# Kernel tuning notes

Measured on AMD Instinct MI355X. Metric: run time of the kernel, lower is better.

Reference implementation:

```python
import jax, jax.numpy as jnp
import numpy as np

T, H, I, E, K, G, TG = 8192, 2048, 1024, 64, 8, 8, 4
ROUTED_SCALE = 2.5


def setup_inputs() -> dict:
    key = jax.random.key(0)
    ks = jax.random.split(key, 7)
    s = 0.02  # weight init scale
    return {
        "hidden_states": jax.random.normal(ks[0], (T, H), jnp.float32),
        "gate_w": jax.random.normal(ks[1], (E, H), jnp.float32) * s,
        "e_bias": jax.random.normal(ks[2], (E,), jnp.float32) * s,
        "w_gate_up": jax.random.normal(ks[3], (E, H, 2 * I), jnp.float32) * s,
        "w_down": jax.random.normal(ks[4], (E, I, H), jnp.float32) * s,
        "shared_gate_up": jax.random.normal(ks[5], (H, 2 * I), jnp.float32) * s,
        "shared_down": jax.random.normal(ks[6], (I, H), jnp.float32) * s,
    }


def silu_and_mul(x):
    g, u = jnp.split(x, 2, axis=-1)
    return jax.nn.silu(g) * u


def grouped_topk(router_logits, e_bias):
    # sigmoid scoring with e_score_correction_bias (DeepSeek-V3 / GLM4-MoE style)
    scores = jax.nn.sigmoid(router_logits)            # [T, E]
    scores_for_choice = scores + e_bias[None, :]
    # group score = sum of top-2 biased scores in each group
    grp = scores_for_choice.reshape(-1, G, E // G)
    group_scores = jax.lax.top_k(grp, 2)[0].sum(-1)   # [T, G]
    _, gidx = jax.lax.top_k(group_scores, TG)         # [T, TG]
    tok = jnp.arange(scores.shape[0])[:, None]
    group_mask = jnp.zeros_like(group_scores, dtype=bool).at[tok, gidx].set(True)
    expert_mask = jnp.repeat(group_mask, E // G, axis=-1)  # [T, E]
    masked = jnp.where(expert_mask, scores_for_choice, -jnp.inf)
    _, topk_ids = jax.lax.top_k(masked, K)            # [T, K]
    # combine weights come from the *unbiased* sigmoid scores
    topk_w = jnp.take_along_axis(scores, topk_ids, axis=-1)
    topk_w = topk_w / jnp.sum(topk_w, axis=-1, keepdims=True)  # renormalize
    return topk_w, topk_ids


def reference(hidden_states, gate_w, e_bias, w_gate_up, w_down,
              shared_gate_up, shared_down):
    x = hidden_states                                  # [T, H]
    # gate runs in fp32
    router_logits = x.astype(jnp.float32) @ gate_w.T   # [T, E]
    topk_w, topk_ids = grouped_topk(router_logits, e_bias)

    # shared expert MLP
    shared_out = silu_and_mul(x @ shared_gate_up) @ shared_down  # [T, H]

    # dense [T, E] combine matrix (top-k sparse in values)
    tok = jnp.arange(x.shape[0])[:, None]
    route = jnp.zeros((x.shape[0], E), x.dtype).at[tok, topk_ids].set(
        topk_w.astype(x.dtype))

    # grouped expert GEMMs via scan over experts (bounds peak memory)
    def body(acc, params):
        w1, w2, rw = params                            # [H,2I], [I,H], [T]
        y = silu_and_mul(x @ w1) @ w2                  # [T, H]
        return acc + rw[:, None] * y, None

    acc0 = jnp.zeros_like(x)
    routed_out, _ = jax.lax.scan(body, acc0, (w_gate_up, w_down, route.T))

    return routed_out * ROUTED_SCALE + shared_out
```

## Files before the change

kernel.cpp:

```cpp
#include <hip/hip_runtime.h>
#include <stdint.h>

#define T_TOK 8192
#define HDIM  2048
#define IDIM  1024
#define NEXP  64
#define KTOP  8
#define TGRP  4
#define TKTOT (T_TOK*KTOP)
#define MAXTILES 1024
#define RSCALE 2.5f

typedef __attribute__((ext_vector_type(8))) short short8;
typedef __attribute__((ext_vector_type(4))) float f32x4;

__device__ __forceinline__ float bf2f(uint16_t u) {
    union { unsigned i; float f; } v; v.i = ((unsigned)u) << 16; return v.f;
}
__device__ __forceinline__ uint16_t f2bf(float f) {
    union { float f; unsigned i; } v; v.f = f;
    unsigned r = (v.i + 0x7FFFu + ((v.i >> 16) & 1u)) >> 16;
    return (uint16_t)r;
}
__device__ __forceinline__ void gload_lds16(const void* g, void* l) {
    __builtin_amdgcn_global_load_lds(
        (const __attribute__((address_space(1))) void*)g,
        (__attribute__((address_space(3))) void*)l, 16, 0, 0);
}
__device__ __forceinline__ int imin(int a, int b) { return a < b ? a : b; }

__global__ __launch_bounds__(256) void k_router(
    const float* __restrict__ x, const float* __restrict__ gw,
    const float* __restrict__ ebias,
    int* __restrict__ topk_ids, float* __restrict__ topk_w,
    int* __restrict__ counts)
{
    __shared__ float xs[16][132];
    __shared__ float wsb[64][133];
    __shared__ float sc[16][65];
    __shared__ float su[16][65];
    const int tid = threadIdx.x;
    const int e = tid & 63;
    const int tg = tid >> 6;
    const long tblk = (long)blockIdx.x * 16;

    float acc0 = 0.f, acc1 = 0.f, acc2 = 0.f, acc3 = 0.f;
    for (int ch = 0; ch < 16; ++ch) {
        const int h0 = ch << 7;
        for (int i = tid; i < 512; i += 256) {
            int r = i >> 5, c4 = (i & 31) << 2;
            float4 v = *(const float4*)(x + (tblk + r) * HDIM + h0 + c4);
            *(float4*)&xs[r][c4] = v;
        }
        for (int i = tid; i < 8192; i += 256) {
            int r = i >> 7, c = i & 127;
            wsb[r][c] = gw[(long)r * HDIM + h0 + c];
        }
        __syncthreads();
        #pragma unroll 8
        for (int hh = 0; hh < 128; ++hh) {
            float wv = wsb[e][hh];
            acc0 += xs[tg][hh] * wv;
            acc1 += xs[tg + 4][hh] * wv;
            acc2 += xs[tg + 8][hh] * wv;
            acc3 += xs[tg + 12][hh] * wv;
        }
        __syncthreads();
    }
    const float be = ebias[e];
    {
        float s;
        s = 1.f / (1.f + expf(-acc0)); su[tg][e] = s;      sc[tg][e] = s + be;
        s = 1.f / (1.f + expf(-acc1)); su[tg + 4][e] = s;  sc[tg + 4][e] = s + be;
        s = 1.f / (1.f + expf(-acc2)); su[tg + 8][e] = s;  sc[tg + 8][e] = s + be;
        s = 1.f / (1.f + expf(-acc3)); su[tg + 12][e] = s; sc[tg + 12][e] = s + be;
    }
    __syncthreads();
    if (tid < 16) {
        const int t = tid;
        float gs[8];
        #pragma unroll
        for (int g = 0; g < 8; ++g) {
            float m1 = -1e30f, m2 = -1e30f;
            #pragma unroll
            for (int j = 0; j < 8; ++j) {
                float v = sc[t][g * 8 + j];
                if (v > m1) { m2 = m1; m1 = v; } else if (v > m2) { m2 = v; }
            }
            gs[g] = m1 + m2;
        }
        int selmask = 0;
        #pragma unroll
        for (int it = 0; it < TGRP; ++it) {
            float best = -1e30f; int bg = 0;
            #pragma unroll
            for (int g = 0; g < 8; ++g)
                if (!((selmask >> g) & 1) && gs[g] > best) { best = gs[g]; bg = g; }
            selmask |= (1 << bg);
        }
        unsigned long long chosen = 0ull;
        int ids[KTOP]; float wv[KTOP]; float wsum = 0.f;
        #pragma unroll
        for (int it = 0; it < KTOP; ++it) {
            float best = -1e30f; int bi = 0;
            for (int ee = 0; ee < 64; ++ee) {
                if (((selmask >> (ee >> 3)) & 1) && !((chosen >> ee) & 1ull)) {
                    float v = sc[t][ee];
                    if (v > best) { best = v; bi = ee; }
                }
            }
            chosen |= (1ull << bi);
            ids[it] = bi; wv[it] = su[t][bi]; wsum += wv[it];
        }
        const float inv = 1.f / wsum;
        #pragma unroll
        for (int k = 0; k < KTOP; ++k) {
            topk_ids[(tblk + t) * KTOP + k] = ids[k];
            topk_w[(tblk + t) * KTOP + k] = wv[k] * inv;
            atomicAdd(&counts[ids[k]], 1);
        }
    }
}

__global__ void k_scan(const int* __restrict__ counts, int* offsets, int* cursor,
                       int* tile_e, int* tile_r0, int* tile_end, int* ntiles)
{
    if (threadIdx.x || blockIdx.x) return;
    int off = 0, nt = 0;
    for (int e = 0; e < NEXP; ++e) {
        offsets[e] = off; cursor[e] = off;
        int c = counts[e];
        for (int m0 = 0; m0 < c; m0 += 128) {
            tile_e[nt] = e; tile_r0[nt] = off + m0; tile_end[nt] = off + c; ++nt;
        }
        off += c;
    }
    *ntiles = nt;
}

__global__ __launch_bounds__(256) void k_scatter(
    const int* __restrict__ topk_ids, int* cursor,
    int* __restrict__ perm_token, int* __restrict__ slot_of)
{
    int i = blockIdx.x * 256 + threadIdx.x;
    if (i >= TKTOT) return;
    int e = topk_ids[i];
    int pos = atomicAdd(&cursor[e], 1);
    perm_token[pos] = i >> 3;
    slot_of[i] = pos;
}

__global__ __launch_bounds__(256) void k_cvt_bf16(
    const float* __restrict__ in, uint16_t* __restrict__ outp, long n4)
{
    long i = (long)blockIdx.x * 256 + threadIdx.x;
    if (i >= n4) return;
    float4 v = *(const float4*)(in + i * 4);
    uint64_t pk = (uint64_t)f2bf(v.x) | ((uint64_t)f2bf(v.y) << 16)
                | ((uint64_t)f2bf(v.z) << 32) | ((uint64_t)f2bf(v.w) << 48);
    *(uint64_t*)(outp + i * 4) = pk;
}

template<bool INTER>
__global__ __launch_bounds__(256) void k_transpose2(
    const float* __restrict__ src, uint16_t* __restrict__ dst,
    int R, int C, long sStride, long dStride)
{
    __shared__ float tile[64][65];
    const int c0 = blockIdx.x << 6, r0 = blockIdx.y << 6, s = blockIdx.z;
    const float* S = src + (long)s * sStride;
    uint16_t* D = dst + (long)s * dStride;
    const int lc = (threadIdx.x & 15) << 2;
    const int lr = threadIdx.x >> 4;
    #pragma unroll
    for (int p = 0; p < 4; ++p) {
        int y = lr + p * 16;
        float4 v = *(const float4*)(S + (long)(r0 + y) * C + c0 + lc);
        tile[y][lc] = v.x; tile[y][lc + 1] = v.y;
        tile[y][lc + 2] = v.z; tile[y][lc + 3] = v.w;
    }
    __syncthreads();
    const int wc = threadIdx.x >> 3;
    const int wx = (threadIdx.x & 7) << 3;
    #pragma unroll
    for (int p = 0; p < 2; ++p) {
        int c = wc + p * 32;
        short8 v;
        #pragma unroll
        for (int j = 0; j < 8; ++j) v[j] = (short)f2bf(tile[wx + j][c]);
        int cg = c0 + c;
        int rd = INTER ? (((cg & (IDIM - 1)) << 1) + (cg >> 10)) : cg;
        *(short8*)(D + (long)rd * R + r0 + wx) = v;
    }
}

template<bool GATEUP, bool ROUTED>
__global__ __launch_bounds__(256) void k_gemm2(
    const uint16_t* __restrict__ A, const uint16_t* __restrict__ Bw,
    void* __restrict__ OutP,
    const int* __restrict__ perm_token,
    const int* __restrict__ tile_e, const int* __restrict__ tile_r0,
    const int* __restrict__ tile_end, const int* __restrict__ ntiles,
    int* __restrict__ qcur,
    int Kd, long expStride)
{
    __shared__ uint16_t lds[2 * 128 * 64];
    const int tid = threadIdx.x, lane = tid & 63, wid = tid >> 6;

    int aRow[4], aSlotB[4];
    #pragma unroll
    for (int j = 0; j < 4; ++j) {
        int o = wid * 4096 + j * 1024 + lane * 16;
        int r = o >> 7;
        aRow[j] = r;
        aSlotB[j] = ((((o >> 4) & 7) ^ (r & 7)) << 4);
    }

    const int wm = wid >> 1, wn = wid & 1;
    const int rA = wm * 64 + (lane & 15);
    const int rB = wn * 64 + (lane & 15);
    const int kc = lane >> 4;
    const int swz = lane & 7;
    const int es0 = ((kc) ^ swz) << 4;
    const int es1 = ((4 + kc) ^ swz) << 4;
    char* const ldsb = (char*)lds;
    const int nK = Kd >> 6;

    const int ntl = ROUTED ? ntiles[0] : 0;
    const int nitems = ntl << 4;
    __shared__ int s_item;

    for (;;) {
        int row0, end, n0; const uint16_t* Bbase;
        if (ROUTED) {
            __syncthreads();
            if (tid == 0) s_item = atomicAdd(qcur, 1);
            __syncthreads();
            const int it = s_item;
            if (it >= nitems) break;
            const int tIdx = it >> 4;
            n0 = (it & 15) << 7;
            row0 = tile_r0[tIdx]; end = tile_end[tIdx];
            Bbase = Bw + (long)tile_e[tIdx] * expStride;
        } else {
            row0 = (blockIdx.x >> 4) << 7; end = row0 + 128;
            n0 = (blockIdx.x & 15) << 7;
            Bbase = Bw;
        }

        const uint16_t* pa[4]; const uint16_t* pb[4];
        #pragma unroll
        for (int j = 0; j < 4; ++j) {
            int s = row0 + aRow[j];
            if (ROUTED) s = imin(s, end - 1);
            long grow = (GATEUP && ROUTED) ? (long)perm_token[s] : (long)s;
            pa[j] = A + grow * Kd + (aSlotB[j] >> 1);
            pb[j] = Bbase + (long)(n0 + aRow[j]) * Kd + (aSlotB[j] >> 1);
        }

        f32x4 acc[4][4];
        #pragma unroll
        for (int i = 0; i < 4; ++i)
            #pragma unroll
            for (int j = 0; j < 4; ++j) {
                f32x4 z = {0.f, 0.f, 0.f, 0.f};
                acc[i][j] = z;
            }

        for (int kt = 0; kt < nK; ++kt) {
            #pragma unroll
            for (int j = 0; j < 4; ++j)
                gload_lds16(pa[j], ldsb + wid * 4096 + j * 1024);
            #pragma unroll
            for (int j = 0; j < 4; ++j)
                gload_lds16(pb[j], ldsb + 16384 + wid * 4096 + j * 1024);
            #pragma unroll
            for (int j = 0; j < 4; ++j) { pa[j] += 64; pb[j] += 64; }
            __syncthreads();
            short8 af[4], bfr[4];
            #pragma unroll
            for (int f = 0; f < 4; ++f)
                af[f] = *(const short8*)(ldsb + (rA + f * 16) * 128 + es0);
            #pragma unroll
            for (int f = 0; f < 4; ++f)
                bfr[f] = *(const short8*)(ldsb + 16384 + (rB + f * 16) * 128 + es0);
            #pragma unroll
            for (int fm = 0; fm < 4; ++fm)
                #pragma unroll
                for (int fn = 0; fn < 4; ++fn)
                    acc[fm][fn] = __builtin_amdgcn_mfma_f32_16x16x32_bf16(
                        af[fm], bfr[fn], acc[fm][fn], 0, 0, 0);
            #pragma unroll
            for (int f = 0; f < 4; ++f)
                af[f] = *(const short8*)(ldsb + (rA + f * 16) * 128 + es1);
            #pragma unroll
            for (int f = 0; f < 4; ++f)
                bfr[f] = *(const short8*)(ldsb + 16384 + (rB + f * 16) * 128 + es1);
            #pragma unroll
            for (int fm = 0; fm < 4; ++fm)
                #pragma unroll
                for (int fn = 0; fn < 4; ++fn)
                    acc[fm][fn] = __builtin_amdgcn_mfma_f32_16x16x32_bf16(
                        af[fm], bfr[fn], acc[fm][fn], 0, 0, 0);
            __syncthreads();
        }

        const int colb = n0 + wn * 64 + (lane & 15);
        const int rowb = row0 + wm * 64 + (kc << 2);
        if (GATEUP) {
            uint16_t* Oact = (uint16_t*)OutP;
            const bool evenl = ((lane & 1) == 0);
            #pragma unroll
            for (int fm = 0; fm < 4; ++fm)
                #pragma unroll
                for (int fn = 0; fn < 4; ++fn) {
                    f32x4 v = acc[fm][fn];
                    #pragma unroll
                    for (int r = 0; r < 4; ++r) {
                        float g = v[r];
                        float u = __shfl_xor(g, 1, 64);
                        int row = rowb + fm * 16 + r;
                        if (evenl && (!ROUTED || row < end)) {
                            int j = (colb + fn * 16) >> 1;
                            float sg = g / (1.f + expf(-g));
                            Oact[(long)row * IDIM + j] = f2bf(sg * u);
                        }
                    }
                }
        } else if (ROUTED) {
            uint16_t* Y = (uint16_t*)OutP;
            #pragma unroll
            for (int fm = 0; fm < 4; ++fm)
                #pragma unroll
                for (int fn = 0; fn < 4; ++fn) {
                    f32x4 v = acc[fm][fn];
                    #pragma unroll
                    for (int r = 0; r < 4; ++r) {
                        int row = rowb + fm * 16 + r;
                        if (row < end)
                            Y[(long)row * HDIM + colb + fn * 16] = f2bf(v[r]);
                    }
                }
        } else {
            float* O = (float*)OutP;
            #pragma unroll
            for (int fm = 0; fm < 4; ++fm)
                #pragma unroll
                for (int fn = 0; fn < 4; ++fn) {
                    f32x4 v = acc[fm][fn];
                    #pragma unroll
                    for (int r = 0; r < 4; ++r) {
                        int row = rowb + fm * 16 + r;
                        O[(long)row * HDIM + colb + fn * 16] = v[r];
                    }
                }
        }
        if (!ROUTED) break;
    }
}

__global__ __launch_bounds__(256) void k_combine(
    float* __restrict__ out, const uint16_t* __restrict__ ybuf,
    const int* __restrict__ slot_of, const float* __restrict__ topk_w)
{
    __shared__ int sl[KTOP];
    __shared__ float sw[KTOP];
    const int t = blockIdx.x, tid = threadIdx.x;
    if (tid < KTOP) {
        sl[tid] = slot_of[t * KTOP + tid];
        sw[tid] = topk_w[t * KTOP + tid] * RSCALE;
    }
    __syncthreads();
    const int h0 = tid << 3;
    float* orow = out + (long)t * HDIM + h0;
    float4 v0 = *(const float4*)(orow);
    float4 v1 = *(const float4*)(orow + 4);
    float a[8] = { v0.x, v0.y, v0.z, v0.w, v1.x, v1.y, v1.z, v1.w };
    #pragma unroll
    for (int k = 0; k < KTOP; ++k) {
        const uint16_t* yr = ybuf + (long)sl[k] * HDIM + h0;
        short8 y = *(const short8*)yr;
        float w = sw[k];
        #pragma unroll
        for (int j = 0; j < 8; ++j)
            a[j] += w * bf2f((uint16_t)y[j]);
    }
    v0.x = a[0]; v0.y = a[1]; v0.z = a[2]; v0.w = a[3];
    v1.x = a[4]; v1.y = a[5]; v1.z = a[6]; v1.w = a[7];
    *(float4*)(orow) = v0;
    *(float4*)(orow + 4) = v1;
}

extern "C" void kernel_launch(void* const* d_in, const int* in_sizes, int n_in,
                              void* d_out, int out_size, void* d_ws, size_t ws_size,
                              hipStream_t stream)
{
    const float* x  = (const float*)d_in[0];
    const float* gw = (const float*)d_in[1];
    const float* eb = (const float*)d_in[2];
    const float* w1 = (const float*)d_in[3];
    const float* w2 = (const float*)d_in[4];
    const float* s1 = (const float*)d_in[5];
    const float* s2 = (const float*)d_in[6];
    float* out = (float*)d_out;
    char* ws = (char*)d_ws;

    size_t off = 0;
    auto take = [&](size_t b) { size_t r = off; off += (b + 255) & ~(size_t)255; return r; };
    const size_t oXBF = take((size_t)T_TOK * HDIM * 2);
    const size_t oACT = take((size_t)TKTOT * IDIM * 2);
    const size_t oASH = take((size_t)T_TOK * IDIM * 2);
    const size_t oW1T = take((size_t)NEXP * 2048 * 2048 * 2);
    const size_t oW2T = take((size_t)NEXP * 2048 * 1024 * 2);
    const size_t oS1T = take((size_t)2048 * 2048 * 2);
    const size_t oS2T = take((size_t)2048 * 1024 * 2);
    const size_t oTKI = take((size_t)TKTOT * 4);
    const size_t oTKW = take((size_t)TKTOT * 4);
    const size_t oSLT = take((size_t)TKTOT * 4);
    const size_t oPRM = take((size_t)TKTOT * 4);
    const size_t oCTL = take(1024);
    const size_t oOFS = take(256);
    const size_t oCUR = take(256);
    const size_t oNT  = take(256);
    const size_t oTE  = take(MAXTILES * 4);
    const size_t oTR  = take(MAXTILES * 4);
    const size_t oTX  = take(MAXTILES * 4);
    (void)ws_size; (void)in_sizes; (void)n_in; (void)out_size;

    uint16_t* xbf  = (uint16_t*)(ws + oXBF);
    uint16_t* act  = (uint16_t*)(ws + oACT);
    uint16_t* ash  = (uint16_t*)(ws + oASH);
    uint16_t* w1t  = (uint16_t*)(ws + oW1T);
    uint16_t* ybuf = (uint16_t*)(ws + oW1T);
    uint16_t* w2t  = (uint16_t*)(ws + oW2T);
    uint16_t* s1t  = (uint16_t*)(ws + oS1T);
    uint16_t* s2t  = (uint16_t*)(ws + oS2T);
    int*   tki  = (int*)(ws + oTKI);
    float* tkw  = (float*)(ws + oTKW);
    int*   slot = (int*)(ws + oSLT);
    int*   prm  = (int*)(ws + oPRM);
    int*   ctl  = (int*)(ws + oCTL);
    int*   ofs  = (int*)(ws + oOFS);
    int*   cur  = (int*)(ws + oCUR);
    int*   nt   = (int*)(ws + oNT);
    int*   te   = (int*)(ws + oTE);
    int*   tr   = (int*)(ws + oTR);
    int*   tx   = (int*)(ws + oTX);

    hipMemsetAsync(ws + oCTL, 0, 1024, stream);

    k_router<<<T_TOK / 16, 256, 0, stream>>>(x, gw, eb, tki, tkw, ctl);
    k_scan<<<1, 1, 0, stream>>>(ctl, ofs, cur, te, tr, tx, nt);
    k_scatter<<<TKTOT / 256, 256, 0, stream>>>(tki, cur, prm, slot);

    k_cvt_bf16<<<(T_TOK * HDIM / 4 + 255) / 256, 256, 0, stream>>>(x, xbf, (long)T_TOK * HDIM / 4);
    k_transpose2<true ><<<dim3(32, 32, NEXP), 256, 0, stream>>>(w1, w1t, 2048, 2048,
        (long)2048 * 2048, (long)2048 * 2048);
    k_transpose2<false><<<dim3(32, 16, NEXP), 256, 0, stream>>>(w2, w2t, 1024, 2048,
        (long)1024 * 2048, (long)2048 * 1024);
    k_transpose2<true ><<<dim3(32, 32, 1), 256, 0, stream>>>(s1, s1t, 2048, 2048, 0, 0);
    k_transpose2<false><<<dim3(32, 16, 1), 256, 0, stream>>>(s2, s2t, 1024, 2048, 0, 0);

    k_gemm2<true, false><<<dim3((T_TOK / 128) * 16), 256, 0, stream>>>(
        xbf, s1t, ash, nullptr, te, tr, tx, nt, nullptr, 2048, 0);
    k_gemm2<true, true><<<dim3(768), 256, 0, stream>>>(
        xbf, w1t, act, prm, te, tr, tx, nt, ctl + 64, 2048, (long)2048 * 2048);
    k_gemm2<false, false><<<dim3((T_TOK / 128) * 16), 256, 0, stream>>>(
        ash, s2t, out, nullptr, te, tr, tx, nt, nullptr, 1024, 0);
    k_gemm2<false, true><<<dim3(768), 256, 0, stream>>>(
        act, w2t, ybuf, nullptr, te, tr, tx, nt, ctl + 65, 1024, (long)2048 * 1024);

    k_combine<<<T_TOK, 256, 0, stream>>>(out, ybuf, slot, tkw);
}
```

Measured before the change: 2.397 ms.

## Rewrite grouped GEMM with 256x256 tiles and a 4-stage LDS pipeline

The GEMM kernel moves from 128x128 tiles with 256 threads and a single LDS buffer to 256x256 tiles with 512 threads (8 waves, each computing 128x64). It adds a 4-deep ring of LDS buffers filled by direct-to-LDS loads three K-steps ahead, with a vmcnt wait and one barrier per step. The routed work list is rebuilt by a parallel wave-scan kernel that orders items by expert, then N-block, then M-tile, to improve weight reuse. The larger tile cuts global traffic per FLOP and hides load latency, but it raises register and LDS pressure (128KB LDS) and wastes more work on partially filled expert tiles. A launch bound of 2 blocks per CU is requested, which that LDS footprint may not allow.

```diff
diff --git a/kernel.cpp b/kernel.cpp
--- a/kernel.cpp
+++ b/kernel.cpp
@@ -8,7 +8,7 @@
 #define KTOP  8
 #define TGRP  4
 #define TKTOT (T_TOK*KTOP)
-#define MAXTILES 1024
+#define MAXITEMS 4096
 #define RSCALE 2.5f
 
 typedef __attribute__((ext_vector_type(8))) short short8;
@@ -122,20 +122,38 @@
     }
 }
 
-__global__ void k_scan(const int* __restrict__ counts, int* offsets, int* cursor,
-                       int* tile_e, int* tile_r0, int* tile_end, int* ntiles)
-{
-    if (threadIdx.x || blockIdx.x) return;
-    int off = 0, nt = 0;
-    for (int e = 0; e < NEXP; ++e) {
-        offsets[e] = off; cursor[e] = off;
-        int c = counts[e];
-        for (int m0 = 0; m0 < c; m0 += 128) {
-            tile_e[nt] = e; tile_r0[nt] = off + m0; tile_end[nt] = off + c; ++nt;
-        }
-        off += c;
-    }
-    *ntiles = nt;
+__global__ __launch_bounds__(64) void k_scan2(
+    const int* __restrict__ counts, int* offsets, int* cursor,
+    int* __restrict__ it_r0, int* __restrict__ it_end,
+    int* __restrict__ it_e, int* __restrict__ it_n0, int* __restrict__ nitems)
+{
+    const int e = threadIdx.x;
+    const int c = counts[e];
+    int pre = c;
+    #pragma unroll
+    for (int d = 1; d < 64; d <<= 1) {
+        int v = __shfl_up(pre, d, 64);
+        if (e >= d) pre += v;
+    }
+    const int offE = pre - c;
+    offsets[e] = offE; cursor[e] = offE;
+    const int ntl = (c + 255) >> 8;
+    int ipre = ntl;
+    #pragma unroll
+    for (int d = 1; d < 64; d <<= 1) {
+        int v = __shfl_up(ipre, d, 64);
+        if (e >= d) ipre += v;
+    }
+    const int ibase = (ipre - ntl) * 8;
+    for (int p = 0; p < 8; ++p)
+        for (int t = 0; t < ntl; ++t) {
+            int idx = ibase + p * ntl + t;
+            it_r0[idx] = offE + t * 256;
+            it_end[idx] = offE + c;
+            it_e[idx] = e;
+            it_n0[idx] = p << 8;
+        }
+    if (e == 63) *nitems = ibase + ntl * 8;
 }
 
 __global__ __launch_bounds__(256) void k_scatter(
@@ -195,163 +213,153 @@
 }
 
 template<bool GATEUP, bool ROUTED>
-__global__ __launch_bounds__(256) void k_gemm2(
+__global__ __launch_bounds__(512, 2) void k_gemm3(
     const uint16_t* __restrict__ A, const uint16_t* __restrict__ Bw,
     void* __restrict__ OutP,
     const int* __restrict__ perm_token,
-    const int* __restrict__ tile_e, const int* __restrict__ tile_r0,
-    const int* __restrict__ tile_end, const int* __restrict__ ntiles,
-    int* __restrict__ qcur,
+    const int* __restrict__ it_r0, const int* __restrict__ it_end,
+    const int* __restrict__ it_e, const int* __restrict__ it_n0,
+    const int* __restrict__ nitems, int* __restrict__ qcur,
     int Kd, long expStride)
 {
-    __shared__ uint16_t lds[2 * 128 * 64];
+    __shared__ char ldsb[4 * 32768];
+    __shared__ int s_item;
     const int tid = threadIdx.x, lane = tid & 63, wid = tid >> 6;
-
-    int aRow[4], aSlotB[4];
-    #pragma unroll
-    for (int j = 0; j < 4; ++j) {
-        int o = wid * 4096 + j * 1024 + lane * 16;
-        int r = o >> 7;
-        aRow[j] = r;
-        aSlotB[j] = ((((o >> 4) & 7) ^ (r & 7)) << 4);
-    }
-
-    const int wm = wid >> 1, wn = wid & 1;
-    const int rA = wm * 64 + (lane & 15);
-    const int rB = wn * 64 + (lane & 15);
-    const int kc = lane >> 4;
-    const int swz = lane & 7;
-    const int es0 = ((kc) ^ swz) << 4;
-    const int es1 = ((4 + kc) ^ swz) << 4;
-    char* const ldsb = (char*)lds;
-    const int nK = Kd >> 6;
-
-    const int ntl = ROUTED ? ntiles[0] : 0;
-    const int nitems = ntl << 4;
-    __shared__ int s_item;
+    const int wm = wid >> 2, wn = wid & 3;
+
+    const int rchunk = lane >> 2;
+    const int swzS = ((lane & 3) ^ ((lane >> 3) & 3)) << 3;
+    const int swzR = ((lane >> 4) ^ ((lane >> 1) & 3)) << 4;
+    const int aoff = (wm * 128 + (lane & 15)) * 64 + swzR;
+    const int boff = (wn * 64 + (lane & 15)) * 64 + swzR;
+    const int ldst0 = (wid * 2) * 1024;
+    const int ldst1 = (wid * 2 + 1) * 1024;
+
+    const int nSub = Kd >> 5;
+    const int NI = ROUTED ? nitems[0] : 0;
 
     for (;;) {
-        int row0, end, n0; const uint16_t* Bbase;
+        int row0, end, n0; long eoff;
         if (ROUTED) {
             __syncthreads();
             if (tid == 0) s_item = atomicAdd(qcur, 1);
             __syncthreads();
             const int it = s_item;
-            if (it >= nitems) break;
-            const int tIdx = it >> 4;
-            n0 = (it & 15) << 7;
-            row0 = tile_r0[tIdx]; end = tile_end[tIdx];
-            Bbase = Bw + (long)tile_e[tIdx] * expStride;
+            if (it >= NI) break;
+            row0 = it_r0[it]; end = it_end[it]; n0 = it_n0[it];
+            eoff = (long)it_e[it] * expStride;
         } else {
-            row0 = (blockIdx.x >> 4) << 7; end = row0 + 128;
-            n0 = (blockIdx.x & 15) << 7;
-            Bbase = Bw;
-        }
-
-        const uint16_t* pa[4]; const uint16_t* pb[4];
-        #pragma unroll
-        for (int j = 0; j < 4; ++j) {
-            int s = row0 + aRow[j];
-            if (ROUTED) s = imin(s, end - 1);
-            long grow = (GATEUP && ROUTED) ? (long)perm_token[s] : (long)s;
-            pa[j] = A + grow * Kd + (aSlotB[j] >> 1);
-            pb[j] = Bbase + (long)(n0 + aRow[j]) * Kd + (aSlotB[j] >> 1);
-        }
-
-        f32x4 acc[4][4];
-        #pragma unroll
-        for (int i = 0; i < 4; ++i)
-            #pragma unroll
-            for (int j = 0; j < 4; ++j) {
-                f32x4 z = {0.f, 0.f, 0.f, 0.f};
-                acc[i][j] = z;
+            row0 = (int)(blockIdx.x >> 3) << 8;
+            end = row0 + 256;
+            n0 = (int)(blockIdx.x & 7) << 8;
+            eoff = 0;
+        }
+
+        const uint16_t *pA0, *pA1, *pB0, *pB1;
+        {
+            int r0l = (wid * 2) * 16 + rchunk;
+            int r1l = (wid * 2 + 1) * 16 + rchunk;
+            int ra0 = row0 + r0l, ra1 = row0 + r1l;
+            if (ROUTED) { ra0 = imin(ra0, end - 1); ra1 = imin(ra1, end - 1); }
+            long ga0 = (GATEUP && ROUTED) ? (long)perm_token[ra0] : (long)ra0;
+            long ga1 = (GATEUP && ROUTED) ? (long)perm_token[ra1] : (long)ra1;
+            pA0 = A + ga0 * Kd + swzS;
+            pA1 = A + ga1 * Kd + swzS;
+            pB0 = Bw + eoff + (long)(n0 + r0l) * Kd + swzS;
+            pB1 = Bw + eoff + (long)(n0 + r1l) * Kd + swzS;
+        }
+
+        f32x4 acc[8][4];
+        #pragma unroll
+        for (int f = 0; f < 8; ++f)
+            #pragma unroll
+            for (int g = 0; g < 4; ++g) { f32x4 z = {0.f,0.f,0.f,0.f}; acc[f][g] = z; }
+
+        #pragma unroll
+        for (int j = 0; j < 3; ++j) {
+            char* bb = ldsb + j * 32768;
+            gload_lds16(pA0 + (j << 5), bb + ldst0);
+            gload_lds16(pA1 + (j << 5), bb + ldst1);
+            gload_lds16(pB0 + (j << 5), bb + 16384 + ldst0);
+            gload_lds16(pB1 + (j << 5), bb + 16384 + ldst1);
+        }
+
+        for (int j = 0; j < nSub; ++j) {
+            asm volatile("s_waitcnt vmcnt(8)" ::: "memory");
+            __builtin_amdgcn_s_barrier();
+            if (j + 3 < nSub) {
+                const int js = j + 3;
+                char* bb = ldsb + (js & 3) * 32768;
+                gload_lds16(pA0 + (js << 5), bb + ldst0);
+                gload_lds16(pA1 + (js << 5), bb + ldst1);
+                gload_lds16(pB0 + (js << 5), bb + 16384 + ldst0);
+                gload_lds16(pB1 + (js << 5), bb + 16384 + ldst1);
             }
-
-        for (int kt = 0; kt < nK; ++kt) {
-            #pragma unroll
-            for (int j = 0; j < 4; ++j)
-                gload_lds16(pa[j], ldsb + wid * 4096 + j * 1024);
-            #pragma unroll
-            for (int j = 0; j < 4; ++j)
-                gload_lds16(pb[j], ldsb + 16384 + wid * 4096 + j * 1024);
-            #pragma unroll
-            for (int j = 0; j < 4; ++j) { pa[j] += 64; pb[j] += 64; }
-            __syncthreads();
-            short8 af[4], bfr[4];
-            #pragma unroll
-            for (int f = 0; f < 4; ++f)
-                af[f] = *(const short8*)(ldsb + (rA + f * 16) * 128 + es0);
-            #pragma unroll
-            for (int f = 0; f < 4; ++f)
-                bfr[f] = *(const short8*)(ldsb + 16384 + (rB + f * 16) * 128 + es0);
-            #pragma unroll
-            for (int fm = 0; fm < 4; ++fm)
+            const char* bb = ldsb + (j & 3) * 32768;
+            short8 av[8], bv[4];
+            #pragma unroll
+            for (int f = 0; f < 8; ++f)
+                av[f] = *(const short8*)(bb + aoff + f * 1024);
+            #pragma unroll
+            for (int g = 0; g < 4; ++g)
+                bv[g] = *(const short8*)(bb + 16384 + boff + g * 1024);
+            __builtin_amdgcn_s_setprio(1);
+            #pragma unroll
+            for (int f = 0; f < 8; ++f)
                 #pragma unroll
-                for (int fn = 0; fn < 4; ++fn)
-                    acc[fm][fn] = __builtin_amdgcn_mfma_f32_16x16x32_bf16(
-                        af[fm], bfr[fn], acc[fm][fn], 0, 0, 0);
-            #pragma unroll
-            for (int f = 0; f < 4; ++f)
-                af[f] = *(const short8*)(ldsb + (rA + f * 16) * 128 + es1);
-            #pragma unroll
-            for (int f = 0; f < 4; ++f)
-                bfr[f] = *(const short8*)(ldsb + 16384 + (rB + f * 16) * 128 + es1);
-            #pragma unroll
-            for (int fm = 0; fm < 4; ++fm)
-                #pragma unroll
-                for (int fn = 0; fn < 4; ++fn)
-                    acc[fm][fn] = __builtin_amdgcn_mfma_f32_16x16x32_bf16(
-                        af[fm], bfr[fn], acc[fm][fn], 0, 0, 0);
-            __syncthreads();
+                for (int g = 0; g < 4; ++g)
+                    acc[f][g] = __builtin_amdgcn_mfma_f32_16x16x32_bf16(
+                        av[f], bv[g], acc[f][g], 0, 0, 0);
+            __builtin_amdgcn_s_setprio(0);
         }
 
         const int colb = n0 + wn * 64 + (lane & 15);
-        const int rowb = row0 + wm * 64 + (kc << 2);
+        const int rowbase = row0 + wm * 128 + ((lane >> 4) << 2);
         if (GATEUP) {
             uint16_t* Oact = (uint16_t*)OutP;
             const bool evenl = ((lane & 1) == 0);
             #pragma unroll
-            for (int fm = 0; fm < 4; ++fm)
+            for (int f = 0; f < 8; ++f)
                 #pragma unroll
-                for (int fn = 0; fn < 4; ++fn) {
-                    f32x4 v = acc[fm][fn];
+                for (int g = 0; g < 4; ++g) {
+                    f32x4 v = acc[f][g];
                     #pragma unroll
                     for (int r = 0; r < 4; ++r) {
-                        float g = v[r];
-                        float u = __shfl_xor(g, 1, 64);
-                        int row = rowb + fm * 16 + r;
+                        float gg = v[r];
+                        float uu = __shfl_xor(gg, 1, 64);
+                        int row = rowbase + f * 16 + r;
                         if (evenl && (!ROUTED || row < end)) {
-                            int j = (colb + fn * 16) >> 1;
-                            float sg = g / (1.f + expf(-g));
-                            Oact[(long)row * IDIM + j] = f2bf(sg * u);
+                            int jcol = (colb + g * 16) >> 1;
+                            float sg = gg / (1.f + __expf(-gg));
+                            Oact[(long)row * IDIM + jcol] = f2bf(sg * uu);
                         }
                     }
                 }
         } else if (ROUTED) {
             uint16_t* Y = (uint16_t*)OutP;
             #pragma unroll
-            for (int fm = 0; fm < 4; ++fm)
+            for (int f = 0; f < 8; ++f)
                 #pragma unroll
-                for (int fn = 0; fn < 4; ++fn) {
-                    f32x4 v = acc[fm][fn];
+                for (int g = 0; g < 4; ++g) {
+                    f32x4 v = acc[f][g];
                     #pragma unroll
                     for (int r = 0; r < 4; ++r) {
-                        int row = rowb + fm * 16 + r;
+                        int row = rowbase + f * 16 + r;
                         if (row < end)
-                            Y[(long)row * HDIM + colb + fn * 16] = f2bf(v[r]);
+                            Y[(long)row * HDIM + colb + g * 16] = f2bf(v[r]);
                     }
                 }
         } else {
             float* O = (float*)OutP;
             #pragma unroll
-            for (int fm = 0; fm < 4; ++fm)
+            for (int f = 0; f < 8; ++f)
                 #pragma unroll
-                for (int fn = 0; fn < 4; ++fn) {
-                    f32x4 v = acc[fm][fn];
+                for (int g = 0; g < 4; ++g) {
+                    f32x4 v = acc[f][g];
                     #pragma unroll
                     for (int r = 0; r < 4; ++r) {
-                        int row = rowb + fm * 16 + r;
-                        O[(long)row * HDIM + colb + fn * 16] = v[r];
+                        int row = rowbase + f * 16 + r;
+                        O[(long)row * HDIM + colb + g * 16] = v[r];
                     }
                 }
         }
@@ -422,9 +430,10 @@
     const size_t oOFS = take(256);
     const size_t oCUR = take(256);
     const size_t oNT  = take(256);
-    const size_t oTE  = take(MAXTILES * 4);
-    const size_t oTR  = take(MAXTILES * 4);
-    const size_t oTX  = take(MAXTILES * 4);
+    const size_t oIR  = take(MAXITEMS * 4);
+    const size_t oIE  = take(MAXITEMS * 4);
+    const size_t oIX  = take(MAXITEMS * 4);
+    const size_t oIN  = take(MAXITEMS * 4);
     (void)ws_size; (void)in_sizes; (void)n_in; (void)out_size;
 
     uint16_t* xbf  = (uint16_t*)(ws + oXBF);
@@ -443,14 +452,15 @@
     int*   ofs  = (int*)(ws + oOFS);
     int*   cur  = (int*)(ws + oCUR);
     int*   nt   = (int*)(ws + oNT);
-    int*   te   = (int*)(ws + oTE);
-    int*   tr   = (int*)(ws + oTR);
-    int*   tx   = (int*)(ws + oTX);
+    int*   ir0  = (int*)(ws + oIR);
+    int*   iend = (int*)(ws + oIE);
+    int*   ie   = (int*)(ws + oIX);
+    int*   in0  = (int*)(ws + oIN);
 
     hipMemsetAsync(ws + oCTL, 0, 1024, stream);
 
     k_router<<<T_TOK / 16, 256, 0, stream>>>(x, gw, eb, tki, tkw, ctl);
-    k_scan<<<1, 1, 0, stream>>>(ctl, ofs, cur, te, tr, tx, nt);
+    k_scan2<<<1, 64, 0, stream>>>(ctl, ofs, cur, ir0, iend, ie, in0, nt);
     k_scatter<<<TKTOT / 256, 256, 0, stream>>>(tki, cur, prm, slot);
 
     k_cvt_bf16<<<(T_TOK * HDIM / 4 + 255) / 256, 256, 0, stream>>>(x, xbf, (long)T_TOK * HDIM / 4);
@@ -461,14 +471,14 @@
     k_transpose2<true ><<<dim3(32, 32, 1), 256, 0, stream>>>(s1, s1t, 2048, 2048, 0, 0);
     k_transpose2<false><<<dim3(32, 16, 1), 256, 0, stream>>>(s2, s2t, 1024, 2048, 0, 0);
 
-    k_gemm2<true, false><<<dim3((T_TOK / 128) * 16), 256, 0, stream>>>(
-        xbf, s1t, ash, nullptr, te, tr, tx, nt, nullptr, 2048, 0);
-    k_gemm2<true, true><<<dim3(768), 256, 0, stream>>>(
-        xbf, w1t, act, prm, te, tr, tx, nt, ctl + 64, 2048, (long)2048 * 2048);
-    k_gemm2<false, false><<<dim3((T_TOK / 128) * 16), 256, 0, stream>>>(
-        ash, s2t, out, nullptr, te, tr, tx, nt, nullptr, 1024, 0);
-    k_gemm2<false, true><<<dim3(768), 256, 0, stream>>>(
-        act, w2t, ybuf, nullptr, te, tr, tx, nt, ctl + 65, 1024, (long)2048 * 1024);
+    k_gemm3<true, false><<<dim3(256), 512, 0, stream>>>(
+        xbf, s1t, ash, nullptr, nullptr, nullptr, nullptr, nullptr, nullptr, nullptr, 2048, 0);
+    k_gemm3<true, true><<<dim3(256), 512, 0, stream>>>(
+        xbf, w1t, act, prm, ir0, iend, ie, in0, nt, ctl + 64, 2048, (long)2048 * 2048);
+    k_gemm3<false, false><<<dim3(256), 512, 0, stream>>>(
+        ash, s2t, out, nullptr, nullptr, nullptr, nullptr, nullptr, nullptr, nullptr, 1024, 0);
+    k_gemm3<false, true><<<dim3(256), 512, 0, stream>>>(
+        act, w2t, ybuf, nullptr, ir0, iend, ie, in0, nt, ctl + 65, 1024, (long)2048 * 1024);
 
     k_combine<<<T_TOK, 256, 0, stream>>>(out, ybuf, slot, tkw);
 }
```

Result: faster. 2.314 ms (-3.5%).
